# Kernel optimization log

Hardware: AMD Instinct MI355X
Metric: run time of the kernel (lower is better)

Reference implementation:

```python
import jax, jax.numpy as jnp
import numpy as np

SEQ_LEN, INPUT_SIZE, HIDDEN, LAYERS = 2048, 1024, 2048, 4
SCALE = 0.02  # keep tanh out of full saturation; original uses raw randn


def setup_inputs() -> dict:
    key = jax.random.key(0)
    ks = jax.random.split(key, 6)
    x = jax.random.normal(ks[0], (SEQ_LEN, INPUT_SIZE), dtype=jnp.float32)
    W_h = jax.random.normal(ks[1], (LAYERS, HIDDEN, HIDDEN), dtype=jnp.float32) * SCALE
    W_hh = jax.random.normal(ks[2], (LAYERS - 1, HIDDEN, HIDDEN), dtype=jnp.float32) * SCALE
    W_x = jax.random.normal(ks[3], (HIDDEN, INPUT_SIZE), dtype=jnp.float32) * SCALE
    W_y = jax.random.normal(ks[4], (INPUT_SIZE, HIDDEN), dtype=jnp.float32) * SCALE
    B_h = jnp.zeros((LAYERS, HIDDEN), dtype=jnp.float32)
    B_y = jnp.zeros((INPUT_SIZE,), dtype=jnp.float32)
    return {"x": x, "W_h": W_h, "W_hh": W_hh, "W_x": W_x, "W_y": W_y, "B_h": B_h, "B_y": B_y}


def reference(x, W_h, W_hh, W_x, W_y, B_h, B_y):
    L, H = W_h.shape[0], W_h.shape[1]
    # Precompute input projection for all timesteps: [S, H]
    xin = x @ W_x.T

    def step(h, xt):
        hs = []
        for l in range(L):
            if l == 0:
                hl = jnp.tanh(h[l] @ W_h[l].T + xt + B_h[l])
            else:
                hl = jnp.tanh(h[l] @ W_h[l].T + hs[l - 1] @ W_hh[l - 1].T + B_h[l])
            hs.append(hl)
        h_new = jnp.stack(hs)  # [L, H]
        y = hs[-1] @ W_y.T + B_y  # [input_size]
        return h_new, y

    h0 = jnp.zeros((L, H), dtype=x.dtype)
    h_final, ys = jax.lax.scan(step, h0, xin)
    return ys, h_final
```

## Files before the change

### kernel.cpp

```cpp
#include <hip/hip_runtime.h>
#include <math.h>


typedef unsigned int uint32;
typedef unsigned long long uint64;
typedef _Float16 half2_t __attribute__((ext_vector_type(2)));

#define S_LEN 2048
#define IN_SZ 1024
#define HID   2048
#define NLAY  4
#define NWG   256
#define BLK   512
#define H2    1024
#define SENT  0x7F7F7F7Fu
#define SENT64 0x7F7F7F7F7F7F7F7FULL

#define LD_AGENT64(p) __hip_atomic_load((p), __ATOMIC_RELAXED, __HIP_MEMORY_SCOPE_AGENT)
#define ST_AGENT(p,v) __hip_atomic_store((p), (v), __ATOMIC_RELAXED, __HIP_MEMORY_SCOPE_AGENT)

__device__ __forceinline__ float dot2(uint32 a, uint32 b, float c) {
    return __builtin_amdgcn_fdot2(__builtin_bit_cast(half2_t, a),
                                  __builtin_bit_cast(half2_t, b), c, false);
}
__device__ __forceinline__ uint32 packh2(float x, float y) {
    half2_t h; h.x = (_Float16)x; h.y = (_Float16)y;
    return __builtin_bit_cast(uint32, h);
}
__device__ __forceinline__ float fast_tanh(float x) {
#if __has_builtin(__builtin_amdgcn_exp2f) && __has_builtin(__builtin_amdgcn_rcpf)
    float a = fabsf(x);
    float e = __builtin_amdgcn_exp2f(a * 2.885390081777927f);
    float r = 1.f - 2.f * __builtin_amdgcn_rcpf(e + 1.f);
    return copysignf(r, x);
#else
    return tanhf(x);
#endif
}

__global__ __launch_bounds__(BLK, 2) void rnn_scan(
    const float* __restrict__ Wh,
    const float* __restrict__ Whh,
    const float* __restrict__ xin,
    const float* __restrict__ Bh,
    float* __restrict__ hfin,
    uint32* hist)
{
    __shared__ __align__(16) uint32 sh_own[2][H2];
    __shared__ __align__(16) uint32 sh_prev[2][H2];

    const int g   = blockIdx.x;
    const int l   = g >> 6;
    const int w   = g & 63;
    const int tid = threadIdx.x;
    const int v   = tid >> 6;
    const int k   = tid & 63;
    const int r0  = w * 32 + v * 4;

    uint32 wA[64], wB[64];
    const float4 bh4 = *(const float4*)(Bh + l * HID + r0);

    #pragma unroll
    for (int rr = 0; rr < 4; ++rr) {
        const float* wr = Wh + ((size_t)l * HID + r0 + rr) * HID;
        #pragma unroll
        for (int j = 0; j < 4; ++j) {
            const float* p = wr + 8 * k + 512 * j;
            float4 f0 = *(const float4*)p;
            float4 f1 = *(const float4*)(p + 4);
            wA[16 * rr + 4 * j + 0] = packh2(f0.x, f0.y);
            wA[16 * rr + 4 * j + 1] = packh2(f0.z, f0.w);
            wA[16 * rr + 4 * j + 2] = packh2(f1.x, f1.y);
            wA[16 * rr + 4 * j + 3] = packh2(f1.z, f1.w);
        }
    }
    if (l > 0) {
        #pragma unroll
        for (int rr = 0; rr < 4; ++rr) {
            const float* wr2 = Whh + ((size_t)(l - 1) * HID + r0 + rr) * HID;
            #pragma unroll
            for (int j = 0; j < 4; ++j) {
                const float* p = wr2 + 8 * k + 512 * j;
                float4 f0 = *(const float4*)p;
                float4 f1 = *(const float4*)(p + 4);
                wB[16 * rr + 4 * j + 0] = packh2(f0.x, f0.y);
                wB[16 * rr + 4 * j + 1] = packh2(f0.z, f0.w);
                wB[16 * rr + 4 * j + 2] = packh2(f1.x, f1.y);
                wB[16 * rr + 4 * j + 3] = packh2(f1.z, f1.w);
            }
        }
    }

    uint32* histL = hist + (size_t)l * S_LEN * H2;
    uint32* histP = hist + (size_t)(l - 1) * S_LEN * H2;
    const bool needPrev = (l > 0);

    for (int t = 0; t < S_LEN; ++t) {
        const int  p       = t & 1;
        const bool needOwn = (t > 0);

        float4 xv = make_float4(0.f, 0.f, 0.f, 0.f);
        if (l == 0 && k == 0) xv = *(const float4*)(xin + (size_t)t * HID + r0);

        ((uint64*)sh_own [p])[tid] = SENT64;
        ((uint64*)sh_prev[p])[tid] = SENT64;

        asm volatile("s_waitcnt lgkmcnt(0)" ::: "memory");
        __builtin_amdgcn_s_barrier();

        __builtin_amdgcn_s_setprio(0);
        {
            bool dO = !needOwn, dP = !needPrev;
            const size_t tOwn = (size_t)(needOwn ? t - 1 : 0) * H2;
            const uint64* pO = (const uint64*)(histL + tOwn) + tid;
            const uint64* pP = (const uint64*)(histP + (size_t)t * H2) + tid;
            int it = 0;
            while (!(dO & dP)) {
                if (!dP) { uint64 b = LD_AGENT64(pP);
                    if (b != SENT64) { ((uint64*)sh_prev[p])[tid] = b; dP = true; } }
                if (!dO) { uint64 a = LD_AGENT64(pO);
                    if (a != SENT64) { ((uint64*)sh_own[p])[tid] = a; dO = true; } }
                if (dO & dP) break;
                if (it == 0)      __builtin_amdgcn_s_sleep(2);
                else if (it == 1) __builtin_amdgcn_s_sleep(8);
                else              __builtin_amdgcn_s_sleep(16);
                ++it;
            }
        }
        __builtin_amdgcn_s_setprio(1);

        float acc0 = 0.f, acc1 = 0.f, acc2 = 0.f, acc3 = 0.f;

        if (needPrev) {
            uint4 gv[4];
            for (;;) {
                bool bad = false;
                #pragma unroll
                for (int c = 0; c < 4; ++c) {
                    gv[c] = ((const uint4*)sh_prev[p])[k + 64 * c];
                    bad |= (gv[c].x == SENT) | (gv[c].y == SENT) |
                           (gv[c].z == SENT) | (gv[c].w == SENT);
                }
                if (!bad) break;
                __builtin_amdgcn_s_sleep(1);
                asm volatile("" ::: "memory");
            }
            #pragma unroll
            for (int c = 0; c < 4; ++c) {
                acc0 = dot2(wB[4 * c + 0], gv[c].x, acc0);
                acc0 = dot2(wB[4 * c + 1], gv[c].y, acc0);
                acc0 = dot2(wB[4 * c + 2], gv[c].z, acc0);
                acc0 = dot2(wB[4 * c + 3], gv[c].w, acc0);
                acc1 = dot2(wB[16 + 4 * c + 0], gv[c].x, acc1);
                acc1 = dot2(wB[16 + 4 * c + 1], gv[c].y, acc1);
                acc1 = dot2(wB[16 + 4 * c + 2], gv[c].z, acc1);
                acc1 = dot2(wB[16 + 4 * c + 3], gv[c].w, acc1);
                acc2 = dot2(wB[32 + 4 * c + 0], gv[c].x, acc2);
                acc2 = dot2(wB[32 + 4 * c + 1], gv[c].y, acc2);
                acc2 = dot2(wB[32 + 4 * c + 2], gv[c].z, acc2);
                acc2 = dot2(wB[32 + 4 * c + 3], gv[c].w, acc2);
                acc3 = dot2(wB[48 + 4 * c + 0], gv[c].x, acc3);
                acc3 = dot2(wB[48 + 4 * c + 1], gv[c].y, acc3);
                acc3 = dot2(wB[48 + 4 * c + 2], gv[c].z, acc3);
                acc3 = dot2(wB[48 + 4 * c + 3], gv[c].w, acc3);
            }
        }

        if (needOwn) {
            uint4 hv[4];
            for (;;) {
                bool bad = false;
                #pragma unroll
                for (int c = 0; c < 4; ++c) {
                    hv[c] = ((const uint4*)sh_own[p])[k + 64 * c];
                    bad |= (hv[c].x == SENT) | (hv[c].y == SENT) |
                           (hv[c].z == SENT) | (hv[c].w == SENT);
                }
                if (!bad) break;
                __builtin_amdgcn_s_sleep(1);
                asm volatile("" ::: "memory");
            }
            #pragma unroll
            for (int c = 0; c < 4; ++c) {
                acc0 = dot2(wA[4 * c + 0], hv[c].x, acc0);
                acc0 = dot2(wA[4 * c + 1], hv[c].y, acc0);
                acc0 = dot2(wA[4 * c + 2], hv[c].z, acc0);
                acc0 = dot2(wA[4 * c + 3], hv[c].w, acc0);
                acc1 = dot2(wA[16 + 4 * c + 0], hv[c].x, acc1);
                acc1 = dot2(wA[16 + 4 * c + 1], hv[c].y, acc1);
                acc1 = dot2(wA[16 + 4 * c + 2], hv[c].z, acc1);
                acc1 = dot2(wA[16 + 4 * c + 3], hv[c].w, acc1);
                acc2 = dot2(wA[32 + 4 * c + 0], hv[c].x, acc2);
                acc2 = dot2(wA[32 + 4 * c + 1], hv[c].y, acc2);
                acc2 = dot2(wA[32 + 4 * c + 2], hv[c].z, acc2);
                acc2 = dot2(wA[32 + 4 * c + 3], hv[c].w, acc2);
                acc3 = dot2(wA[48 + 4 * c + 0], hv[c].x, acc3);
                acc3 = dot2(wA[48 + 4 * c + 1], hv[c].y, acc3);
                acc3 = dot2(wA[48 + 4 * c + 2], hv[c].z, acc3);
                acc3 = dot2(wA[48 + 4 * c + 3], hv[c].w, acc3);
            }
        }

        #pragma unroll
        for (int off = 32; off > 0; off >>= 1) {
            acc0 += __shfl_xor(acc0, off, 64);
            acc1 += __shfl_xor(acc1, off, 64);
            acc2 += __shfl_xor(acc2, off, 64);
            acc3 += __shfl_xor(acc3, off, 64);
        }

        if (k == 0) {
            float h0 = fast_tanh(acc0 + bh4.x + (l == 0 ? xv.x : 0.f));
            float h1 = fast_tanh(acc1 + bh4.y + (l == 0 ? xv.y : 0.f));
            float h2 = fast_tanh(acc2 + bh4.z + (l == 0 ? xv.z : 0.f));
            float h3 = fast_tanh(acc3 + bh4.w + (l == 0 ? xv.w : 0.f));
            uint64 hw = (uint64)packh2(h0, h1) | ((uint64)packh2(h2, h3) << 32);
            ST_AGENT((uint64*)&histL[(size_t)t * H2 + (r0 >> 1)], hw);
            if (t == S_LEN - 1) {
                hfin[l * HID + r0]     = h0;
                hfin[l * HID + r0 + 1] = h1;
                hfin[l * HID + r0 + 2] = h2;
                hfin[l * HID + r0 + 3] = h3;
            }
        }
    }
}

__global__ __launch_bounds__(256) void gemm_xin(
    const float* __restrict__ A, const float* __restrict__ B,
    float* __restrict__ C, int M, int N, int K)
{
    __shared__ float As[32][65];
    __shared__ float Bs[32][65];

    const int tid = threadIdx.x;
    const int tx = tid & 15, ty = tid >> 4;
    const int i0 = blockIdx.y * 64;
    const int j0 = blockIdx.x * 64;

    float acc[4][4] = {};

    for (int k0 = 0; k0 < K; k0 += 32) {
        #pragma unroll
        for (int ld = tid; ld < 64 * 32; ld += 256) {
            const int r = ld >> 5, kk = ld & 31;
            As[kk][r] = A[(size_t)(i0 + r) * K + k0 + kk];
            Bs[kk][r] = B[(size_t)(j0 + r) * K + k0 + kk];
        }
        __syncthreads();
        #pragma unroll
        for (int kk = 0; kk < 32; ++kk) {
            float a[4], b[4];
            #pragma unroll
            for (int u = 0; u < 4; ++u) a[u] = As[kk][ty * 4 + u];
            #pragma unroll
            for (int u = 0; u < 4; ++u) b[u] = Bs[kk][tx * 4 + u];
            #pragma unroll
            for (int u = 0; u < 4; ++u)
                #pragma unroll
                for (int q = 0; q < 4; ++q)
                    acc[u][q] += a[u] * b[q];
        }
        __syncthreads();
    }
    #pragma unroll
    for (int u = 0; u < 4; ++u)
        #pragma unroll
        for (int q = 0; q < 4; ++q)
            C[(size_t)(i0 + ty * 4 + u) * N + j0 + tx * 4 + q] = acc[u][q];
}

__global__ __launch_bounds__(256) void gemm_out(
    const uint32* __restrict__ A2, const float* __restrict__ B,
    const float* __restrict__ bias, float* __restrict__ C)
{
    __shared__ float As[32][65];
    __shared__ float Bs[32][65];

    const int tid = threadIdx.x;
    const int tx = tid & 15, ty = tid >> 4;
    const int i0 = blockIdx.y * 64;
    const int j0 = blockIdx.x * 64;

    float acc[4][4] = {};

    for (int k0 = 0; k0 < HID; k0 += 32) {
        #pragma unroll
        for (int ld = tid; ld < 1024; ld += 256) {
            const int r = ld >> 4, kk2 = ld & 15;
            half2_t h = __builtin_bit_cast(half2_t,
                A2[(size_t)(i0 + r) * H2 + (k0 >> 1) + kk2]);
            As[2 * kk2][r]     = (float)h.x;
            As[2 * kk2 + 1][r] = (float)h.y;
        }
        #pragma unroll
        for (int ld = tid; ld < 2048; ld += 256) {
            const int rn = ld >> 5, kk = ld & 31;
            Bs[kk][rn] = B[(size_t)(j0 + rn) * HID + k0 + kk];
        }
        __syncthreads();
        #pragma unroll
        for (int kk = 0; kk < 32; ++kk) {
            float a[4], b[4];
            #pragma unroll
            for (int u = 0; u < 4; ++u) a[u] = As[kk][ty * 4 + u];
            #pragma unroll
            for (int u = 0; u < 4; ++u) b[u] = Bs[kk][tx * 4 + u];
            #pragma unroll
            for (int u = 0; u < 4; ++u)
                #pragma unroll
                for (int q = 0; q < 4; ++q)
                    acc[u][q] += a[u] * b[q];
        }
        __syncthreads();
    }
    #pragma unroll
    for (int u = 0; u < 4; ++u)
        #pragma unroll
        for (int q = 0; q < 4; ++q) {
            const int i = i0 + ty * 4 + u;
            const int j = j0 + tx * 4 + q;
            C[(size_t)i * IN_SZ + j] = acc[u][q] + bias[j];
        }
}

extern "C" void kernel_launch(void* const* d_in, const int* in_sizes, int n_in,
                              void* d_out, int out_size, void* d_ws, size_t ws_size,
                              hipStream_t stream) {
    const float* x   = (const float*)d_in[0];
    const float* Wh  = (const float*)d_in[1];
    const float* Whh = (const float*)d_in[2];
    const float* Wx  = (const float*)d_in[3];
    const float* Wy  = (const float*)d_in[4];
    const float* Bh  = (const float*)d_in[5];
    const float* By  = (const float*)d_in[6];

    float* out  = (float*)d_out;
    float* hfin = out + (size_t)S_LEN * IN_SZ;

    float*  xin  = (float*)d_ws;
    uint32* hist = (uint32*)d_ws + (size_t)S_LEN * HID;

    hipMemsetAsync(hist, 0x7F, (size_t)NLAY * S_LEN * H2 * sizeof(uint32), stream);

    gemm_xin<<<dim3(HID / 64, S_LEN / 64), 256, 0, stream>>>(
        x, Wx, xin, S_LEN, HID, IN_SZ);

    rnn_scan<<<NWG, BLK, 0, stream>>>(Wh, Whh, xin, Bh, hfin, hist);

    gemm_out<<<dim3(IN_SZ / 64, S_LEN / 64), 256, 0, stream>>>(
        hist + (size_t)3 * S_LEN * H2, Wy, By, out);
}
```

Baseline: 5.879 ms.

## Broadcast own-layer hidden state via replicated 4-slot ring buffers

```diff
diff --git a/kernel.cpp b/kernel.cpp
--- a/kernel.cpp
+++ b/kernel.cpp
@@ -13,8 +13,10 @@
 #define NWG   256
 #define BLK   512
 #define H2    1024
+#define NREP  8
 #define SENT  0x7F7F7F7Fu
 #define SENT64 0x7F7F7F7F7F7F7F7FULL
+#define GUARD_MAX 4096u
 
 #define LD_AGENT64(p) __hip_atomic_load((p), __ATOMIC_RELAXED, __HIP_MEMORY_SCOPE_AGENT)
 #define ST_AGENT(p,v) __hip_atomic_store((p), (v), __ATOMIC_RELAXED, __HIP_MEMORY_SCOPE_AGENT)
@@ -44,7 +46,8 @@
     const float* __restrict__ xin,
     const float* __restrict__ Bh,
     float* __restrict__ hfin,
-    uint32* hist)
+    uint32* hist,
+    uint64* ring)
 {
     __shared__ __align__(16) uint32 sh_own[2][H2];
     __shared__ __align__(16) uint32 sh_prev[2][H2];
@@ -56,6 +59,7 @@
     const int v   = tid >> 6;
     const int k   = tid & 63;
     const int r0  = w * 32 + v * 4;
+    const int uo  = w * 8 + v;
 
     uint32 wA[64], wB[64];
     const float4 bh4 = *(const float4*)(Bh + l * HID + r0);
@@ -94,6 +98,8 @@
     uint32* histL = hist + (size_t)l * S_LEN * H2;
     uint32* histP = hist + (size_t)(l - 1) * S_LEN * H2;
     const bool needPrev = (l > 0);
+    uint64* ringL = ring + (size_t)l * NREP * 4 * 512;
+    const uint64* ringC = ringL + (size_t)(w & 7) * 4 * 512;
 
     for (int t = 0; t < S_LEN; ++t) {
         const int  p       = t & 1;
@@ -102,6 +108,13 @@
         float4 xv = make_float4(0.f, 0.f, 0.f, 0.f);
         if (l == 0 && k == 0) xv = *(const float4*)(xin + (size_t)t * HID + r0);
 
+        if (k == 0) {
+            const int cs = (t + 1) & 3;
+            #pragma unroll
+            for (int r = 0; r < NREP; ++r)
+                ST_AGENT(&ringL[(r * 4 + cs) * 512 + uo], SENT64);
+        }
+
         ((uint64*)sh_own [p])[tid] = SENT64;
         ((uint64*)sh_prev[p])[tid] = SENT64;
 
@@ -111,16 +124,17 @@
         __builtin_amdgcn_s_setprio(0);
         {
             bool dO = !needOwn, dP = !needPrev;
-            const size_t tOwn = (size_t)(needOwn ? t - 1 : 0) * H2;
-            const uint64* pO = (const uint64*)(histL + tOwn) + tid;
+            const uint64* pO = ringC + (size_t)((t - 1) & 3) * 512 + tid;
             const uint64* pP = (const uint64*)(histP + (size_t)t * H2) + tid;
             int it = 0;
+            uint32 guard = 0;
             while (!(dO & dP)) {
                 if (!dP) { uint64 b = LD_AGENT64(pP);
                     if (b != SENT64) { ((uint64*)sh_prev[p])[tid] = b; dP = true; } }
                 if (!dO) { uint64 a = LD_AGENT64(pO);
                     if (a != SENT64) { ((uint64*)sh_own[p])[tid] = a; dO = true; } }
                 if (dO & dP) break;
+                if (++guard > GUARD_MAX) break;
                 if (it == 0)      __builtin_amdgcn_s_sleep(2);
                 else if (it == 1) __builtin_amdgcn_s_sleep(8);
                 else              __builtin_amdgcn_s_sleep(16);
@@ -133,6 +147,7 @@
 
         if (needPrev) {
             uint4 gv[4];
+            uint32 guard = 0;
             for (;;) {
                 bool bad = false;
                 #pragma unroll
@@ -141,7 +156,7 @@
                     bad |= (gv[c].x == SENT) | (gv[c].y == SENT) |
                            (gv[c].z == SENT) | (gv[c].w == SENT);
                 }
-                if (!bad) break;
+                if (!bad || ++guard > GUARD_MAX) break;
                 __builtin_amdgcn_s_sleep(1);
                 asm volatile("" ::: "memory");
             }
@@ -168,6 +183,7 @@
 
         if (needOwn) {
             uint4 hv[4];
+            uint32 guard = 0;
             for (;;) {
                 bool bad = false;
                 #pragma unroll
@@ -176,7 +192,7 @@
                     bad |= (hv[c].x == SENT) | (hv[c].y == SENT) |
                            (hv[c].z == SENT) | (hv[c].w == SENT);
                 }
-                if (!bad) break;
+                if (!bad || ++guard > GUARD_MAX) break;
                 __builtin_amdgcn_s_sleep(1);
                 asm volatile("" ::: "memory");
             }
@@ -215,6 +231,11 @@
             float h2 = fast_tanh(acc2 + bh4.z + (l == 0 ? xv.z : 0.f));
             float h3 = fast_tanh(acc3 + bh4.w + (l == 0 ? xv.w : 0.f));
             uint64 hw = (uint64)packh2(h0, h1) | ((uint64)packh2(h2, h3) << 32);
+            asm volatile("s_waitcnt vmcnt(0)" ::: "memory");
+            const int ss = t & 3;
+            #pragma unroll
+            for (int r = 0; r < NREP; ++r)
+                ST_AGENT(&ringL[(r * 4 + ss) * 512 + uo], hw);
             ST_AGENT((uint64*)&histL[(size_t)t * H2 + (r0 >> 1)], hw);
             if (t == S_LEN - 1) {
                 hfin[l * HID + r0]     = h0;
@@ -341,12 +362,16 @@
     float*  xin  = (float*)d_ws;
     uint32* hist = (uint32*)d_ws + (size_t)S_LEN * HID;
 
+    uint64* ring = (uint64*)d_out;
+    const size_t ring_bytes = (size_t)NLAY * NREP * 4 * 512 * sizeof(uint64);
+
     hipMemsetAsync(hist, 0x7F, (size_t)NLAY * S_LEN * H2 * sizeof(uint32), stream);
+    hipMemsetAsync(ring, 0x7F, ring_bytes, stream);
 
     gemm_xin<<<dim3(HID / 64, S_LEN / 64), 256, 0, stream>>>(
         x, Wx, xin, S_LEN, HID, IN_SZ);
 
-    rnn_scan<<<NWG, BLK, 0, stream>>>(Wh, Whh, xin, Bh, hfin, hist);
+    rnn_scan<<<NWG, BLK, 0, stream>>>(Wh, Whh, xin, Bh, hfin, hist, ring);
 
     gemm_out<<<dim3(IN_SZ / 64, S_LEN / 64), 256, 0, stream>>>(
         hist + (size_t)3 * S_LEN * H2, Wy, By, out);
```

After: 6.573 ms. +11.8%, slower.
